# Optimization experiments

Hardware: AMD Instinct MI355X
Metric: run time of the kernel (lower is better)

## Reference

```python
import jax, jax.numpy as jnp
import numpy as np

B = 8192
H = 1024            # hidden_size
A = 512             # alphabet_size
S = 2               # sequence_length
D_IN = A * S        # 1024, gate input dim
D1, D2 = H // 2, H // 3   # decoder dims: 512, 341
TEMP = 1.0


def _linear_params(key, out_d, in_d):
    kw, kb = jax.random.split(key)
    lim = 1.0 / np.sqrt(in_d)
    W = jax.random.uniform(kw, (out_d, in_d), minval=-lim, maxval=lim, dtype=jnp.float32)
    b = jax.random.uniform(kb, (out_d,), minval=-lim, maxval=lim, dtype=jnp.float32)
    return W, b


def setup_inputs() -> dict:
    key = jax.random.key(0)
    ks = jax.random.split(key, 16)
    inp = {
        'x': jax.random.normal(ks[0], (B, D_IN), dtype=jnp.float32),
        'h': jax.random.normal(ks[1], (B, H), dtype=jnp.float32),
        'c': jax.random.normal(ks[2], (B, H), dtype=jnp.float32),
    }
    names = [('W_fi', 'b_fi', H, D_IN), ('W_fh', 'b_fh', H, H),
             ('W_ii', 'b_ii', H, D_IN), ('W_ih', 'b_ih', H, H),
             ('W_si', 'b_si', H, D_IN), ('W_sh', 'b_sh', H, H),
             ('W_oi', 'b_oi', H, D_IN), ('W_oh', 'b_oh', H, H),
             ('W_d1', 'b_d1', D1, H), ('W_d2', 'b_d2', D2, D1),
             ('W_d3', 'b_d3', A, D2)]
    for k, (wn, bn, od, idm) in zip(ks[3:3 + len(names)], names):
        W, b = _linear_params(k, od, idm)
        inp[wn] = W
        inp[bn] = b
    return inp


def reference(x, h, c,
              W_fi, b_fi, W_fh, b_fh,
              W_ii, b_ii, W_ih, b_ih,
              W_si, b_si, W_sh, b_sh,
              W_oi, b_oi, W_oh, b_oh,
              W_d1, b_d1, W_d2, b_d2, W_d3, b_d3):
    def lin(v, W, b):
        return v @ W.T + b

    f = jax.nn.sigmoid(lin(x, W_fi, b_fi) + lin(h, W_fh, b_fh))
    i = jax.nn.sigmoid(lin(x, W_ii, b_ii) + lin(h, W_ih, b_ih))
    s = jnp.tanh(lin(x, W_si, b_si) + lin(h, W_sh, b_sh))
    o = jax.nn.sigmoid(lin(x, W_oi, b_oi) + lin(h, W_oh, b_oh))
    c_new = c * f + i * s
    h_new = o * jnp.tanh(c_new)
    d = jnp.tanh(lin(h_new, W_d1, b_d1))
    d = jnp.tanh(lin(d, W_d2, b_d2))
    d = jax.nn.softmax(lin(d, W_d3, b_d3) / TEMP, axis=-1)
    return h_new, d
```

## Files before the change

kernel.cpp:

```cpp
#include <hip/hip_runtime.h>
#include <cstdint>
#include <cstddef>


typedef _Float16 half_t;
typedef _Float16 half8 __attribute__((ext_vector_type(8)));
typedef _Float16 half4v __attribute__((ext_vector_type(4)));
typedef float float4v __attribute__((ext_vector_type(4)));

#define GLD_LDS16(gptr, lptr)                                                  \
  __builtin_amdgcn_global_load_lds(                                            \
      (const __attribute__((address_space(1))) void*)(gptr),                   \
      (__attribute__((address_space(3))) void*)(lptr), 16, 0, 0)

__device__ __forceinline__ float fsig(float x) {
  return 1.0f / (1.0f + __expf(-x));
}
__device__ __forceinline__ float ftanh_(float x) {
  const float e = __expf(2.0f * x);
  return 1.0f - 2.0f / (e + 1.0f);
}

__global__ __launch_bounds__(512, 2) void gemm_gates(const half_t* __restrict__ A,
                                                     const half_t* __restrict__ Bw,
                                                     const float* __restrict__ bias,
                                                     const float* __restrict__ cin,
                                                     float* __restrict__ hout,
                                                     half_t* __restrict__ h2f) {
  constexpr int K = 2048;
  constexpr int NT = 64;
  __shared__ alignas(16) half_t As[3][256 * 32];
  __shared__ alignas(16) half_t Bs[3][256 * 32];
  const int tid = threadIdx.x;
  const int lane = tid & 63;
  const int wave = tid >> 6;
  const int m = lane & 15;
  const int q = lane >> 4;
  const int ks = (q ^ ((m >> 1) & 3)) << 3;
  const int wm = (wave >> 2) << 7;
  const int wn = (wave & 3) << 6;

  const int bid = blockIdx.x;
  const int xcd = bid & 7;
  const int l = bid >> 3;
  const size_t tile_n = (size_t)((xcd << 1) | (l & 1)) << 8;
  const size_t tile_m = (size_t)(l >> 1) << 8;

  const int ci0 = tid, ci1 = tid + 512;
  const int r0 = ci0 >> 2, k0s = (ci0 & 3) ^ ((r0 >> 1) & 3);
  const int r1 = ci1 >> 2, k1s = (ci1 & 3) ^ ((r1 >> 1) & 3);
  const half_t* Ag0 = A + (tile_m + r0) * (size_t)K + k0s * 8;
  const half_t* Ag1 = A + (tile_m + r1) * (size_t)K + k1s * 8;
  const half_t* Bg0 = Bw + (tile_n + r0) * (size_t)K + k0s * 8;
  const half_t* Bg1 = Bw + (tile_n + r1) * (size_t)K + k1s * 8;
  const int p0 = ci0 * 16, p1 = ci1 * 16;

  GLD_LDS16(Ag0, (char*)As[0] + p0);
  GLD_LDS16(Ag1, (char*)As[0] + p1);
  GLD_LDS16(Bg0, (char*)Bs[0] + p0);
  GLD_LDS16(Bg1, (char*)Bs[0] + p1);
  GLD_LDS16(Ag0 + 32, (char*)As[1] + p0);
  GLD_LDS16(Ag1 + 32, (char*)As[1] + p1);
  GLD_LDS16(Bg0 + 32, (char*)Bs[1] + p0);
  GLD_LDS16(Bg1 + 32, (char*)Bs[1] + p1);
  asm volatile("s_waitcnt vmcnt(4)" ::: "memory");
  __builtin_amdgcn_s_barrier();
  __builtin_amdgcn_sched_barrier(0);

  float4v acc[8][4] = {};
  int bc = 0;
  for (int t = 0; t < NT; ++t) {
    const half_t* as = As[bc];
    const half_t* bs = Bs[bc];
    const int bst = (bc + 2 >= 3) ? bc - 1 : bc + 2;
    const size_t koff = (size_t)(t + 2) * 32;
    half8 af[4], bf[4];
#pragma unroll
    for (int i = 0; i < 4; ++i)
      af[i] = *(const half8*)(as + (wm + i * 16 + m) * 32 + ks);
#pragma unroll
    for (int j = 0; j < 4; ++j)
      bf[j] = *(const half8*)(bs + (wn + j * 16 + m) * 32 + ks);
    if (t < NT - 2) {
      GLD_LDS16(Ag0 + koff, (char*)As[bst] + p0);
      GLD_LDS16(Ag1 + koff, (char*)As[bst] + p1);
    }
    __builtin_amdgcn_s_barrier();
    asm volatile("s_waitcnt lgkmcnt(0)" ::: "memory");
    __builtin_amdgcn_sched_barrier(0);
    __builtin_amdgcn_s_setprio(1);
#pragma unroll
    for (int i = 0; i < 4; ++i)
#pragma unroll
      for (int j = 0; j < 4; ++j)
        acc[i][j] = __builtin_amdgcn_mfma_f32_16x16x32_f16(af[i], bf[j],
                                                           acc[i][j], 0, 0, 0);
    __builtin_amdgcn_s_setprio(0);
    __builtin_amdgcn_s_barrier();
    __builtin_amdgcn_sched_barrier(0);
    half8 ag[4];
#pragma unroll
    for (int i = 0; i < 4; ++i)
      ag[i] = *(const half8*)(as + (wm + 64 + i * 16 + m) * 32 + ks);
    if (t < NT - 2) {
      GLD_LDS16(Bg0 + koff, (char*)Bs[bst] + p0);
      GLD_LDS16(Bg1 + koff, (char*)Bs[bst] + p1);
    }
    __builtin_amdgcn_s_barrier();
    asm volatile("s_waitcnt lgkmcnt(0)" ::: "memory");
    __builtin_amdgcn_sched_barrier(0);
    __builtin_amdgcn_s_setprio(1);
#pragma unroll
    for (int i = 0; i < 4; ++i)
#pragma unroll
      for (int j = 0; j < 4; ++j)
        acc[4 + i][j] = __builtin_amdgcn_mfma_f32_16x16x32_f16(
            ag[i], bf[j], acc[4 + i][j], 0, 0, 0);
    __builtin_amdgcn_s_setprio(0);
    if (t < NT - 2) {
      asm volatile("s_waitcnt vmcnt(4)" ::: "memory");
    } else if (t == NT - 2) {
      asm volatile("s_waitcnt vmcnt(0)" ::: "memory");
    }
    __builtin_amdgcn_s_barrier();
    __builtin_amdgcn_sched_barrier(0);
    bc = (bc + 1 == 3) ? 0 : bc + 1;
  }

  const int nwave = (int)tile_n + wn;
  const int u = ((nwave >> 6) << 4) + m;
  const int rtb = (int)((tile_m + wm) >> 4);
  const int ubase = (u >> 5) * 512 + ((u >> 3) & 3) * 128 + (u & 7);
  float bg[4];
#pragma unroll
  for (int g = 0; g < 4; ++g) bg[g] = bias[nwave + g * 16 + m];
#pragma unroll
  for (int i = 0; i < 8; ++i) {
#pragma unroll
    for (int r = 0; r < 4; ++r) {
      const size_t row = tile_m + wm + q * 4 + i * 16 + r;
      const size_t off = row * 1024 + u;
      const float F = fsig(acc[i][0][r] + bg[0]);
      const float I = fsig(acc[i][1][r] + bg[1]);
      const float S = ftanh_(acc[i][2][r] + bg[2]);
      const float O = fsig(acc[i][3][r] + bg[3]);
      const float cn = cin[off] * F + I * S;
      const float hn = O * ftanh_(cn);
      hout[off] = hn;
      h2f[(size_t)(rtb + i) * 16384 + ubase + (q * 4 + r) * 8] = (half_t)hn;
    }
  }
}

__global__ __launch_bounds__(512, 2) void fused_decoder(
    const half_t* __restrict__ h2f,
    const half_t* __restrict__ W1f,
    const float* __restrict__ b1,
    const half_t* __restrict__ W2f,
    const float* __restrict__ b2,
    const half_t* __restrict__ W3f,
    const float* __restrict__ b3,
    float* __restrict__ out) {
  __shared__ alignas(16) half_t A1s[2 * 16384];
  __shared__ alignas(16) half_t A2s[2 * 8192];
  __shared__ alignas(16) half_t A3s[2 * 6144];
  float* LOGL = (float*)A1s;

  const int tid = threadIdx.x;
  const int lane = tid & 63;
  const int w = tid >> 6;
  const int m = lane & 15;
  const int q = lane >> 4;
  const int b = blockIdx.x;

  const half_t* src = h2f + (size_t)b * 32768;
#pragma unroll
  for (int it = 0; it < 8; ++it)
    GLD_LDS16(src + (it * 512 + tid) * 8, (char*)A1s + (it * 512 + tid) * 16);
  asm volatile("s_waitcnt vmcnt(0)" ::: "memory");
  __syncthreads();

  {
    float4v acc[2][4] = {};
    const half_t* w1 = W1f + (size_t)(w * 4) * 16384 + lane * 8;
#pragma unroll 2
    for (int c = 0; c < 32; ++c) {
      half8 wf[4], af[2];
#pragma unroll
      for (int j = 0; j < 4; ++j)
        wf[j] = *(const half8*)(w1 + j * 16384 + c * 512);
#pragma unroll
      for (int rt = 0; rt < 2; ++rt)
        af[rt] = *(const half8*)(A1s + rt * 16384 + c * 512 + q * 128 + m * 8);
#pragma unroll
      for (int rt = 0; rt < 2; ++rt)
#pragma unroll
        for (int j = 0; j < 4; ++j)
          acc[rt][j] = __builtin_amdgcn_mfma_f32_16x16x32_f16(af[rt], wf[j],
                                                              acc[rt][j], 0, 0, 0);
    }
#pragma unroll
    for (int j = 0; j < 4; ++j) {
      const int col = w * 64 + j * 16 + m;
      const float bv = b1[col];
      const int cb = (col >> 5) * 512 + ((col >> 3) & 3) * 128 + (col & 7);
#pragma unroll
      for (int rt = 0; rt < 2; ++rt)
#pragma unroll
        for (int r = 0; r < 4; ++r)
          A2s[rt * 8192 + cb + (q * 4 + r) * 8] = (half_t)ftanh_(acc[rt][j][r] + bv);
    }
  }
  __syncthreads();

  {
    float4v acc[2][3] = {};
    const half_t* w2 = W2f + (size_t)(w * 3) * 8192 + lane * 8;
#pragma unroll 2
    for (int c = 0; c < 16; ++c) {
      half8 wf[3], af[2];
#pragma unroll
      for (int j = 0; j < 3; ++j)
        wf[j] = *(const half8*)(w2 + j * 8192 + c * 512);
#pragma unroll
      for (int rt = 0; rt < 2; ++rt)
        af[rt] = *(const half8*)(A2s + rt * 8192 + c * 512 + q * 128 + m * 8);
#pragma unroll
      for (int rt = 0; rt < 2; ++rt)
#pragma unroll
        for (int j = 0; j < 3; ++j)
          acc[rt][j] = __builtin_amdgcn_mfma_f32_16x16x32_f16(af[rt], wf[j],
                                                              acc[rt][j], 0, 0, 0);
    }
#pragma unroll
    for (int j = 0; j < 3; ++j) {
      const int col = w * 48 + j * 16 + m;
      const float bv = b2[col];
      const int cb = (col >> 5) * 512 + ((col >> 3) & 3) * 128 + (col & 7);
#pragma unroll
      for (int rt = 0; rt < 2; ++rt)
#pragma unroll
        for (int r = 0; r < 4; ++r)
          A3s[rt * 6144 + cb + (q * 4 + r) * 8] = (half_t)ftanh_(acc[rt][j][r] + bv);
    }
  }
  __syncthreads();

  {
    float4v acc[2][4] = {};
    const half_t* w3 = W3f + (size_t)(w * 4) * 6144 + lane * 8;
#pragma unroll 2
    for (int c = 0; c < 12; ++c) {
      half8 wf[4], af[2];
#pragma unroll
      for (int j = 0; j < 4; ++j)
        wf[j] = *(const half8*)(w3 + j * 6144 + c * 512);
#pragma unroll
      for (int rt = 0; rt < 2; ++rt)
        af[rt] = *(const half8*)(A3s + rt * 6144 + c * 512 + q * 128 + m * 8);
#pragma unroll
      for (int rt = 0; rt < 2; ++rt)
#pragma unroll
        for (int j = 0; j < 4; ++j)
          acc[rt][j] = __builtin_amdgcn_mfma_f32_16x16x32_f16(af[rt], wf[j],
                                                              acc[rt][j], 0, 0, 0);
    }
#pragma unroll
    for (int j = 0; j < 4; ++j) {
      const int col = w * 64 + j * 16 + m;
      const float bv = b3[col];
#pragma unroll
      for (int rt = 0; rt < 2; ++rt)
#pragma unroll
        for (int r = 0; r < 4; ++r)
          LOGL[(rt * 16 + q * 4 + r) * 512 + col] = acc[rt][j][r] + bv;
    }
  }
  __syncthreads();

#pragma unroll
  for (int rr = 0; rr < 4; ++rr) {
    const int row = w * 4 + rr;
    const float4v* srcv = (const float4v*)(LOGL + row * 512);
    const float4v v0 = srcv[lane * 2];
    const float4v v1 = srcv[lane * 2 + 1];
    float mx = fmaxf(fmaxf(fmaxf(v0.x, v0.y), fmaxf(v0.z, v0.w)),
                     fmaxf(fmaxf(v1.x, v1.y), fmaxf(v1.z, v1.w)));
#pragma unroll
    for (int off = 32; off > 0; off >>= 1) mx = fmaxf(mx, __shfl_xor(mx, off, 64));
    const float e0 = __expf(v0.x - mx), e1 = __expf(v0.y - mx);
    const float e2 = __expf(v0.z - mx), e3 = __expf(v0.w - mx);
    const float e4 = __expf(v1.x - mx), e5 = __expf(v1.y - mx);
    const float e6 = __expf(v1.z - mx), e7 = __expf(v1.w - mx);
    float sum = ((e0 + e1) + (e2 + e3)) + ((e4 + e5) + (e6 + e7));
#pragma unroll
    for (int off = 32; off > 0; off >>= 1) sum += __shfl_xor(sum, off, 64);
    const float inv = 1.0f / sum;
    float4v o0, o1;
    o0.x = e0 * inv; o0.y = e1 * inv; o0.z = e2 * inv; o0.w = e3 * inv;
    o1.x = e4 * inv; o1.y = e5 * inv; o1.z = e6 * inv; o1.w = e7 * inv;
    float4v* dst = (float4v*)(out + ((size_t)b * 32 + row) * 512);
    dst[lane * 2] = o0;
    dst[lane * 2 + 1] = o1;
  }
}

__global__ void prep_pack(const float* __restrict__ x, const float* __restrict__ h,
                          const float* __restrict__ Wfi, const float* __restrict__ Wfh,
                          const float* __restrict__ Wii, const float* __restrict__ Wih,
                          const float* __restrict__ Wsi, const float* __restrict__ Wsh,
                          const float* __restrict__ Woi, const float* __restrict__ Woh,
                          half_t* __restrict__ xh, half_t* __restrict__ wall) {
  const int bid = blockIdx.x;
  const float* src;
  half_t* dst;
  size_t idx;
  if (bid < 16384) {
    idx = ((size_t)bid * 256 + threadIdx.x) * 4;
    const size_t b = idx >> 11;
    const int col = (int)(idx & 2047);
    src = (col < 1024) ? (x + b * 1024 + col) : (h + b * 1024 + (col - 1024));
    dst = xh + idx;
  } else {
    idx = ((size_t)(bid - 16384) * 256 + threadIdx.x) * 4;
    const int n = (int)(idx >> 11);
    const int col = (int)(idx & 2047);
    const int g = (n >> 4) & 3;
    const size_t u = (size_t)(((n >> 6) << 4) | (n & 15));
    const float* Wi = (g == 0) ? Wfi : (g == 1) ? Wii : (g == 2) ? Wsi : Woi;
    const float* Wh = (g == 0) ? Wfh : (g == 1) ? Wih : (g == 2) ? Wsh : Woh;
    src = (col < 1024) ? (Wi + u * 1024 + col) : (Wh + u * 1024 + (col - 1024));
    dst = wall + idx;
  }
  const float4v v = *(const float4v*)src;
  half4v o;
  o.x = (half_t)v.x; o.y = (half_t)v.y; o.z = (half_t)v.z; o.w = (half_t)v.w;
  *(half4v*)dst = o;
}

__global__ void prep_small(const float* __restrict__ Wd1, const float* __restrict__ Wd2,
                           const float* __restrict__ Wd3, const float* __restrict__ bd2,
                           const float* __restrict__ bfi, const float* __restrict__ bfh,
                           const float* __restrict__ bii, const float* __restrict__ bih,
                           const float* __restrict__ bsi, const float* __restrict__ bsh,
                           const float* __restrict__ boi, const float* __restrict__ boh,
                           half_t* __restrict__ WD1, half_t* __restrict__ WD2h,
                           half_t* __restrict__ WD3h, float* __restrict__ BALL,
                           float* __restrict__ BD2) {
  const int bid = blockIdx.x;
  const int tid = threadIdx.x;
  if (bid < 512) {
    const size_t i4 = ((size_t)bid * 256 + tid) * 4;
    const int col = (int)(i4 >> 10);
    const int k0 = (int)(i4 & 1023);
    const float4v v = *(const float4v*)(Wd1 + i4);
    half4v o;
    o.x = (half_t)v.x; o.y = (half_t)v.y; o.z = (half_t)v.z; o.w = (half_t)v.w;
    const size_t fa = (size_t)(col >> 4) * 16384 + (k0 >> 5) * 512 +
                      ((k0 >> 3) & 3) * 128 + (col & 15) * 8 + (k0 & 7);
    *(half4v*)(WD1 + fa) = o;
  } else if (bid < 704) {
    const size_t i4 = ((size_t)(bid - 512) * 256 + tid) * 4;
    const int col = (int)(i4 >> 9);
    const int k0 = (int)(i4 & 511);
    half4v o;
    if (col < 341) {
      const float4v v = *(const float4v*)(Wd2 + (size_t)col * 512 + k0);
      o.x = (half_t)v.x; o.y = (half_t)v.y; o.z = (half_t)v.z; o.w = (half_t)v.w;
    } else {
      o.x = (half_t)0.f; o.y = (half_t)0.f; o.z = (half_t)0.f; o.w = (half_t)0.f;
    }
    const size_t fa = (size_t)(col >> 4) * 8192 + (k0 >> 5) * 512 +
                      ((k0 >> 3) & 3) * 128 + (col & 15) * 8 + (k0 & 7);
    *(half4v*)(WD2h + fa) = o;
  } else if (bid < 896) {
    const size_t i4 = ((size_t)(bid - 704) * 256 + tid) * 4;
    const int col = (int)(i4 / 384);
    const int k0 = (int)(i4 - (size_t)col * 384);
    half4v o;
    o.x = (k0 + 0 < 341) ? (half_t)Wd3[(size_t)col * 341 + k0 + 0] : (half_t)0.f;
    o.y = (k0 + 1 < 341) ? (half_t)Wd3[(size_t)col * 341 + k0 + 1] : (half_t)0.f;
    o.z = (k0 + 2 < 341) ? (half_t)Wd3[(size_t)col * 341 + k0 + 2] : (half_t)0.f;
    o.w = (k0 + 3 < 341) ? (half_t)Wd3[(size_t)col * 341 + k0 + 3] : (half_t)0.f;
    const size_t fa = (size_t)(col >> 4) * 6144 + (k0 >> 5) * 512 +
                      ((k0 >> 3) & 3) * 128 + (col & 15) * 8 + (k0 & 7);
    *(half4v*)(WD3h + fa) = o;
  } else if (bid < 912) {
    const int n = (bid - 896) * 256 + tid;
    const int g = (n >> 4) & 3;
    const int u = ((n >> 6) << 4) | (n & 15);
    const float* bi = (g == 0) ? bfi : (g == 1) ? bii : (g == 2) ? bsi : boi;
    const float* bh = (g == 0) ? bfh : (g == 1) ? bih : (g == 2) ? bsh : boh;
    BALL[n] = bi[u] + bh[u];
  } else {
    const int i = (bid - 912) * 256 + tid;
    if (i < 384) BD2[i] = (i < 341) ? bd2[i] : 0.0f;
  }
}

extern "C" void kernel_launch(void* const* d_in, const int* in_sizes, int n_in,
                              void* d_out, int out_size, void* d_ws, size_t ws_size,
                              hipStream_t stream) {
  const float* x = (const float*)d_in[0];
  const float* h = (const float*)d_in[1];
  const float* c = (const float*)d_in[2];
  const float* Wfi = (const float*)d_in[3];  const float* bfi = (const float*)d_in[4];
  const float* Wfh = (const float*)d_in[5];  const float* bfh = (const float*)d_in[6];
  const float* Wii = (const float*)d_in[7];  const float* bii = (const float*)d_in[8];
  const float* Wih = (const float*)d_in[9];  const float* bih = (const float*)d_in[10];
  const float* Wsi = (const float*)d_in[11]; const float* bsi = (const float*)d_in[12];
  const float* Wsh = (const float*)d_in[13]; const float* bsh = (const float*)d_in[14];
  const float* Woi = (const float*)d_in[15]; const float* boi = (const float*)d_in[16];
  const float* Woh = (const float*)d_in[17]; const float* boh = (const float*)d_in[18];
  const float* Wd1 = (const float*)d_in[19]; const float* bd1 = (const float*)d_in[20];
  const float* Wd2 = (const float*)d_in[21]; const float* bd2 = (const float*)d_in[22];
  const float* Wd3 = (const float*)d_in[23]; const float* bd3 = (const float*)d_in[24];

  char* ws = (char*)d_ws;
  size_t o = 0;
  auto alloc = [&](size_t bytes) {
    size_t cur = o;
    o += (bytes + 255) & ~(size_t)255;
    return cur;
  };
  half_t* XH   = (half_t*)(ws + alloc((size_t)8192 * 2048 * 2));
  half_t* WALL = (half_t*)(ws + alloc((size_t)4096 * 2048 * 2));
  float*  BALL = (float*)(ws + alloc(4096 * 4));
  half_t* WD1  = (half_t*)(ws + alloc((size_t)512 * 1024 * 2));
  half_t* WD2  = (half_t*)(ws + alloc((size_t)384 * 512 * 2));
  float*  BD2  = (float*)(ws + alloc(384 * 4));
  half_t* WD3  = (half_t*)(ws + alloc((size_t)512 * 384 * 2));
  half_t* H2F  = (half_t*)(ws + alloc((size_t)8192 * 1024 * 2));

  float* h_out = (float*)d_out;
  float* d_outp = (float*)d_out + (size_t)8192 * 1024;

  prep_pack<<<24576, 256, 0, stream>>>(x, h, Wfi, Wfh, Wii, Wih, Wsi, Wsh, Woi, Woh,
                                       XH, WALL);
  prep_small<<<914, 256, 0, stream>>>(Wd1, Wd2, Wd3, bd2, bfi, bfh, bii, bih, bsi, bsh,
                                      boi, boh, WD1, WD2, WD3, BALL, BD2);

  gemm_gates<<<512, 512, 0, stream>>>(XH, WALL, BALL, c, h_out, H2F);

  fused_decoder<<<256, 512, 0, stream>>>(H2F, WD1, bd1, WD2, BD2, WD3, bd3, d_outp);
}
```

Measured before the change: 384.3 us.

## Halve decoder rows per block to double grid, and grid-stride the pack kernel

The fused decoder now handles 16 batch rows per block instead of 32. This doubles the grid to 512 blocks, halves LDS use and register accumulators, and raises the occupancy hint to 4 blocks per CU, so all CUs have work. The cost is that each block reloads the full decoder weights for half as many rows, which doubles weight traffic from L2. Separately, the fp32-to-fp16 pack kernel changes from one-shot 24576 blocks to a 2048-block grid-stride loop to cut block launch overhead.

After: 390.8 us. Within noise of the previous version (+1.7%).

```diff
diff --git a/kernel.cpp b/kernel.cpp
--- a/kernel.cpp
+++ b/kernel.cpp
@@ -152,7 +152,7 @@
   }
 }
 
-__global__ __launch_bounds__(512, 2) void fused_decoder(
+__global__ __launch_bounds__(512, 4) void fused_decoder(
     const half_t* __restrict__ h2f,
     const half_t* __restrict__ W1f,
     const float* __restrict__ b1,
@@ -161,9 +161,9 @@
     const half_t* __restrict__ W3f,
     const float* __restrict__ b3,
     float* __restrict__ out) {
-  __shared__ alignas(16) half_t A1s[2 * 16384];
-  __shared__ alignas(16) half_t A2s[2 * 8192];
-  __shared__ alignas(16) half_t A3s[2 * 6144];
+  __shared__ alignas(16) half_t A1s[16384];
+  __shared__ alignas(16) half_t A2s[8192];
+  __shared__ alignas(16) half_t A3s[6144];
   float* LOGL = (float*)A1s;
 
   const int tid = threadIdx.x;
@@ -173,31 +173,26 @@
   const int q = lane >> 4;
   const int b = blockIdx.x;
 
-  const half_t* src = h2f + (size_t)b * 32768;
-#pragma unroll
-  for (int it = 0; it < 8; ++it)
+  const half_t* src = h2f + (size_t)b * 16384;
+#pragma unroll
+  for (int it = 0; it < 4; ++it)
     GLD_LDS16(src + (it * 512 + tid) * 8, (char*)A1s + (it * 512 + tid) * 16);
   asm volatile("s_waitcnt vmcnt(0)" ::: "memory");
   __syncthreads();
 
   {
-    float4v acc[2][4] = {};
+    float4v acc[4] = {};
     const half_t* w1 = W1f + (size_t)(w * 4) * 16384 + lane * 8;
-#pragma unroll 2
+#pragma unroll 4
     for (int c = 0; c < 32; ++c) {
-      half8 wf[4], af[2];
+      half8 wf[4], af;
 #pragma unroll
       for (int j = 0; j < 4; ++j)
         wf[j] = *(const half8*)(w1 + j * 16384 + c * 512);
-#pragma unroll
-      for (int rt = 0; rt < 2; ++rt)
-        af[rt] = *(const half8*)(A1s + rt * 16384 + c * 512 + q * 128 + m * 8);
-#pragma unroll
-      for (int rt = 0; rt < 2; ++rt)
-#pragma unroll
-        for (int j = 0; j < 4; ++j)
-          acc[rt][j] = __builtin_amdgcn_mfma_f32_16x16x32_f16(af[rt], wf[j],
-                                                              acc[rt][j], 0, 0, 0);
+      af = *(const half8*)(A1s + c * 512 + q * 128 + m * 8);
+#pragma unroll
+      for (int j = 0; j < 4; ++j)
+        acc[j] = __builtin_amdgcn_mfma_f32_16x16x32_f16(af, wf[j], acc[j], 0, 0, 0);
     }
 #pragma unroll
     for (int j = 0; j < 4; ++j) {
@@ -205,32 +200,25 @@
       const float bv = b1[col];
       const int cb = (col >> 5) * 512 + ((col >> 3) & 3) * 128 + (col & 7);
 #pragma unroll
-      for (int rt = 0; rt < 2; ++rt)
-#pragma unroll
-        for (int r = 0; r < 4; ++r)
-          A2s[rt * 8192 + cb + (q * 4 + r) * 8] = (half_t)ftanh_(acc[rt][j][r] + bv);
+      for (int r = 0; r < 4; ++r)
+        A2s[cb + (q * 4 + r) * 8] = (half_t)ftanh_(acc[j][r] + bv);
     }
   }
   __syncthreads();
 
   {
-    float4v acc[2][3] = {};
+    float4v acc[3] = {};
     const half_t* w2 = W2f + (size_t)(w * 3) * 8192 + lane * 8;
-#pragma unroll 2
+#pragma unroll 4
     for (int c = 0; c < 16; ++c) {
-      half8 wf[3], af[2];
+      half8 wf[3], af;
 #pragma unroll
       for (int j = 0; j < 3; ++j)
         wf[j] = *(const half8*)(w2 + j * 8192 + c * 512);
-#pragma unroll
-      for (int rt = 0; rt < 2; ++rt)
-        af[rt] = *(const half8*)(A2s + rt * 8192 + c * 512 + q * 128 + m * 8);
-#pragma unroll
-      for (int rt = 0; rt < 2; ++rt)
-#pragma unroll
-        for (int j = 0; j < 3; ++j)
-          acc[rt][j] = __builtin_amdgcn_mfma_f32_16x16x32_f16(af[rt], wf[j],
-                                                              acc[rt][j], 0, 0, 0);
+      af = *(const half8*)(A2s + c * 512 + q * 128 + m * 8);
+#pragma unroll
+      for (int j = 0; j < 3; ++j)
+        acc[j] = __builtin_amdgcn_mfma_f32_16x16x32_f16(af, wf[j], acc[j], 0, 0, 0);
     }
 #pragma unroll
     for (int j = 0; j < 3; ++j) {
@@ -238,49 +226,40 @@
       const float bv = b2[col];
       const int cb = (col >> 5) * 512 + ((col >> 3) & 3) * 128 + (col & 7);
 #pragma unroll
-      for (int rt = 0; rt < 2; ++rt)
-#pragma unroll
-        for (int r = 0; r < 4; ++r)
-          A3s[rt * 6144 + cb + (q * 4 + r) * 8] = (half_t)ftanh_(acc[rt][j][r] + bv);
+      for (int r = 0; r < 4; ++r)
+        A3s[cb + (q * 4 + r) * 8] = (half_t)ftanh_(acc[j][r] + bv);
     }
   }
   __syncthreads();
 
   {
-    float4v acc[2][4] = {};
+    float4v acc[4] = {};
     const half_t* w3 = W3f + (size_t)(w * 4) * 6144 + lane * 8;
-#pragma unroll 2
+#pragma unroll 4
     for (int c = 0; c < 12; ++c) {
-      half8 wf[4], af[2];
+      half8 wf[4], af;
 #pragma unroll
       for (int j = 0; j < 4; ++j)
         wf[j] = *(const half8*)(w3 + j * 6144 + c * 512);
-#pragma unroll
-      for (int rt = 0; rt < 2; ++rt)
-        af[rt] = *(const half8*)(A3s + rt * 6144 + c * 512 + q * 128 + m * 8);
-#pragma unroll
-      for (int rt = 0; rt < 2; ++rt)
-#pragma unroll
-        for (int j = 0; j < 4; ++j)
-          acc[rt][j] = __builtin_amdgcn_mfma_f32_16x16x32_f16(af[rt], wf[j],
-                                                              acc[rt][j], 0, 0, 0);
+      af = *(const half8*)(A3s + c * 512 + q * 128 + m * 8);
+#pragma unroll
+      for (int j = 0; j < 4; ++j)
+        acc[j] = __builtin_amdgcn_mfma_f32_16x16x32_f16(af, wf[j], acc[j], 0, 0, 0);
     }
 #pragma unroll
     for (int j = 0; j < 4; ++j) {
       const int col = w * 64 + j * 16 + m;
       const float bv = b3[col];
 #pragma unroll
-      for (int rt = 0; rt < 2; ++rt)
-#pragma unroll
-        for (int r = 0; r < 4; ++r)
-          LOGL[(rt * 16 + q * 4 + r) * 512 + col] = acc[rt][j][r] + bv;
+      for (int r = 0; r < 4; ++r)
+        LOGL[(q * 4 + r) * 512 + col] = acc[j][r] + bv;
     }
   }
   __syncthreads();
 
 #pragma unroll
-  for (int rr = 0; rr < 4; ++rr) {
-    const int row = w * 4 + rr;
+  for (int rr = 0; rr < 2; ++rr) {
+    const int row = w * 2 + rr;
     const float4v* srcv = (const float4v*)(LOGL + row * 512);
     const float4v v0 = srcv[lane * 2];
     const float4v v1 = srcv[lane * 2 + 1];
@@ -299,43 +278,48 @@
     float4v o0, o1;
     o0.x = e0 * inv; o0.y = e1 * inv; o0.z = e2 * inv; o0.w = e3 * inv;
     o1.x = e4 * inv; o1.y = e5 * inv; o1.z = e6 * inv; o1.w = e7 * inv;
-    float4v* dst = (float4v*)(out + ((size_t)b * 32 + row) * 512);
+    float4v* dst = (float4v*)(out + ((size_t)b * 16 + row) * 512);
     dst[lane * 2] = o0;
     dst[lane * 2 + 1] = o1;
   }
 }
 
-__global__ void prep_pack(const float* __restrict__ x, const float* __restrict__ h,
-                          const float* __restrict__ Wfi, const float* __restrict__ Wfh,
-                          const float* __restrict__ Wii, const float* __restrict__ Wih,
-                          const float* __restrict__ Wsi, const float* __restrict__ Wsh,
-                          const float* __restrict__ Woi, const float* __restrict__ Woh,
-                          half_t* __restrict__ xh, half_t* __restrict__ wall) {
-  const int bid = blockIdx.x;
-  const float* src;
-  half_t* dst;
-  size_t idx;
-  if (bid < 16384) {
-    idx = ((size_t)bid * 256 + threadIdx.x) * 4;
-    const size_t b = idx >> 11;
-    const int col = (int)(idx & 2047);
-    src = (col < 1024) ? (x + b * 1024 + col) : (h + b * 1024 + (col - 1024));
-    dst = xh + idx;
-  } else {
-    idx = ((size_t)(bid - 16384) * 256 + threadIdx.x) * 4;
-    const int n = (int)(idx >> 11);
-    const int col = (int)(idx & 2047);
-    const int g = (n >> 4) & 3;
-    const size_t u = (size_t)(((n >> 6) << 4) | (n & 15));
-    const float* Wi = (g == 0) ? Wfi : (g == 1) ? Wii : (g == 2) ? Wsi : Woi;
-    const float* Wh = (g == 0) ? Wfh : (g == 1) ? Wih : (g == 2) ? Wsh : Woh;
-    src = (col < 1024) ? (Wi + u * 1024 + col) : (Wh + u * 1024 + (col - 1024));
-    dst = wall + idx;
-  }
-  const float4v v = *(const float4v*)src;
-  half4v o;
-  o.x = (half_t)v.x; o.y = (half_t)v.y; o.z = (half_t)v.z; o.w = (half_t)v.w;
-  *(half4v*)dst = o;
+__global__ __launch_bounds__(256) void prep_pack(
+    const float* __restrict__ x, const float* __restrict__ h,
+    const float* __restrict__ Wfi, const float* __restrict__ Wfh,
+    const float* __restrict__ Wii, const float* __restrict__ Wih,
+    const float* __restrict__ Wsi, const float* __restrict__ Wsh,
+    const float* __restrict__ Woi, const float* __restrict__ Woh,
+    half_t* __restrict__ xh, half_t* __restrict__ wall) {
+  constexpr size_t NXH = (size_t)8192 * 2048 / 4;
+  constexpr size_t NTOT = NXH + (size_t)4096 * 2048 / 4;
+  constexpr size_t STRIDE = (size_t)2048 * 256;
+  for (size_t qd = (size_t)blockIdx.x * 256 + threadIdx.x; qd < NTOT;
+       qd += STRIDE) {
+    const float* src;
+    half_t* dst;
+    if (qd < NXH) {
+      const size_t idx = qd * 4;
+      const size_t bb = idx >> 11;
+      const int col = (int)(idx & 2047);
+      src = (col < 1024) ? (x + bb * 1024 + col) : (h + bb * 1024 + (col - 1024));
+      dst = xh + idx;
+    } else {
+      const size_t idx = (qd - NXH) * 4;
+      const int n = (int)(idx >> 11);
+      const int col = (int)(idx & 2047);
+      const int g = (n >> 4) & 3;
+      const size_t u = (size_t)(((n >> 6) << 4) | (n & 15));
+      const float* Wi = (g == 0) ? Wfi : (g == 1) ? Wii : (g == 2) ? Wsi : Woi;
+      const float* Wh = (g == 0) ? Wfh : (g == 1) ? Wih : (g == 2) ? Wsh : Woh;
+      src = (col < 1024) ? (Wi + u * 1024 + col) : (Wh + u * 1024 + (col - 1024));
+      dst = wall + idx;
+    }
+    const float4v v = *(const float4v*)src;
+    half4v o;
+    o.x = (half_t)v.x; o.y = (half_t)v.y; o.z = (half_t)v.z; o.w = (half_t)v.w;
+    *(half4v*)dst = o;
+  }
 }
 
 __global__ void prep_small(const float* __restrict__ Wd1, const float* __restrict__ Wd2,
@@ -435,12 +419,12 @@
   float* h_out = (float*)d_out;
   float* d_outp = (float*)d_out + (size_t)8192 * 1024;
 
-  prep_pack<<<24576, 256, 0, stream>>>(x, h, Wfi, Wfh, Wii, Wih, Wsi, Wsh, Woi, Woh,
-                                       XH, WALL);
+  prep_pack<<<2048, 256, 0, stream>>>(x, h, Wfi, Wfh, Wii, Wih, Wsi, Wsh, Woi, Woh,
+                                      XH, WALL);
   prep_small<<<914, 256, 0, stream>>>(Wd1, Wd2, Wd3, bd2, bfi, bfh, bii, bih, bsi, bsh,
                                       boi, boh, WD1, WD2, WD3, BALL, BD2);
 
   gemm_gates<<<512, 512, 0, stream>>>(XH, WALL, BALL, c, h_out, H2F);
 
-  fused_decoder<<<256, 512, 0, stream>>>(H2F, WD1, bd1, WD2, BD2, WD3, bd3, d_outp);
-}
+  fused_decoder<<<512, 512, 0, stream>>>(H2F, WD1, bd1, WD2, BD2, WD3, bd3, d_outp);
+}
```

## Retile gates GEMM to 256x128 block tiles with 64-deep K stages

Applied to the files above, without the earlier changes.

Changes the fused gate GEMM block tile from 256x256 with K=32 per stage to 256x128 with K=64 per stage. The grid doubles to 1024 blocks, each wave now owns a 64x64 output tile, and the LDS swizzle changes to an XOR over 8 chunks. The loop is split into two K-halves, and the global-to-LDS loads are redistributed across them. The aim is to halve the number of pipeline iterations and barriers and to give more blocks for scheduling. In exchange, each block reuses less data, so operand LDS reads per MFMA go up, and the LDS footprint grows to about 144KB per block.

After: 385.4 us. About the same (+0.3%).

```diff
diff --git a/kernel.cpp b/kernel.cpp
--- a/kernel.cpp
+++ b/kernel.cpp
@@ -28,62 +28,70 @@
                                                      float* __restrict__ hout,
                                                      half_t* __restrict__ h2f) {
   constexpr int K = 2048;
-  constexpr int NT = 64;
-  __shared__ alignas(16) half_t As[3][256 * 32];
-  __shared__ alignas(16) half_t Bs[3][256 * 32];
+  constexpr int NT = 32;
+  __shared__ alignas(16) half_t As[3][256 * 64];
+  __shared__ alignas(16) half_t Bs[3][128 * 64];
   const int tid = threadIdx.x;
   const int lane = tid & 63;
   const int wave = tid >> 6;
   const int m = lane & 15;
   const int q = lane >> 4;
-  const int ks = (q ^ ((m >> 1) & 3)) << 3;
-  const int wm = (wave >> 2) << 7;
-  const int wn = (wave & 3) << 6;
+  const int x0 = ((q) ^ (m & 7)) << 3;
+  const int x1 = ((4 + q) ^ (m & 7)) << 3;
+  const int wm = (wave >> 1) << 6;
+  const int wn = (wave & 1) << 6;
 
   const int bid = blockIdx.x;
   const int xcd = bid & 7;
   const int l = bid >> 3;
-  const size_t tile_n = (size_t)((xcd << 1) | (l & 1)) << 8;
-  const size_t tile_m = (size_t)(l >> 1) << 8;
-
-  const int ci0 = tid, ci1 = tid + 512;
-  const int r0 = ci0 >> 2, k0s = (ci0 & 3) ^ ((r0 >> 1) & 3);
-  const int r1 = ci1 >> 2, k1s = (ci1 & 3) ^ ((r1 >> 1) & 3);
-  const half_t* Ag0 = A + (tile_m + r0) * (size_t)K + k0s * 8;
-  const half_t* Ag1 = A + (tile_m + r1) * (size_t)K + k1s * 8;
-  const half_t* Bg0 = Bw + (tile_n + r0) * (size_t)K + k0s * 8;
-  const half_t* Bg1 = Bw + (tile_n + r1) * (size_t)K + k1s * 8;
-  const int p0 = ci0 * 16, p1 = ci1 * 16;
-
-  GLD_LDS16(Ag0, (char*)As[0] + p0);
-  GLD_LDS16(Ag1, (char*)As[0] + p1);
-  GLD_LDS16(Bg0, (char*)Bs[0] + p0);
-  GLD_LDS16(Bg1, (char*)Bs[0] + p1);
-  GLD_LDS16(Ag0 + 32, (char*)As[1] + p0);
-  GLD_LDS16(Ag1 + 32, (char*)As[1] + p1);
-  GLD_LDS16(Bg0 + 32, (char*)Bs[1] + p0);
-  GLD_LDS16(Bg1 + 32, (char*)Bs[1] + p1);
-  asm volatile("s_waitcnt vmcnt(4)" ::: "memory");
+  const size_t tile_n = (size_t)((xcd << 2) | (l & 3)) << 7;
+  const size_t tile_m = (size_t)(l >> 2) << 8;
+
+  const int r0 = tid >> 3;
+  const int cs = (((tid & 7) ^ (r0 & 7)) << 3);
+  const half_t* Ag0 = A + (tile_m + r0) * (size_t)K + cs;
+  const half_t* Ag1 = Ag0 + (size_t)64 * K;
+  const half_t* Ag2 = Ag0 + (size_t)128 * K;
+  const half_t* Ag3 = Ag0 + (size_t)192 * K;
+  const half_t* Bg0 = Bw + (tile_n + r0) * (size_t)K + cs;
+  const half_t* Bg1 = Bg0 + (size_t)64 * K;
+  const int pa0 = tid * 16, pa1 = pa0 + 8192, pa2 = pa0 + 16384, pa3 = pa0 + 24576;
+  const int pb0 = tid * 16, pb1 = pb0 + 8192;
+
+  GLD_LDS16(Ag0, (char*)As[0] + pa0);
+  GLD_LDS16(Ag1, (char*)As[0] + pa1);
+  GLD_LDS16(Bg0, (char*)Bs[0] + pb0);
+  GLD_LDS16(Ag2, (char*)As[0] + pa2);
+  GLD_LDS16(Ag3, (char*)As[0] + pa3);
+  GLD_LDS16(Bg1, (char*)Bs[0] + pb1);
+  GLD_LDS16(Ag0 + 64, (char*)As[1] + pa0);
+  GLD_LDS16(Ag1 + 64, (char*)As[1] + pa1);
+  GLD_LDS16(Bg0 + 64, (char*)Bs[1] + pb0);
+  GLD_LDS16(Ag2 + 64, (char*)As[1] + pa2);
+  GLD_LDS16(Ag3 + 64, (char*)As[1] + pa3);
+  GLD_LDS16(Bg1 + 64, (char*)Bs[1] + pb1);
+  asm volatile("s_waitcnt vmcnt(6)" ::: "memory");
   __builtin_amdgcn_s_barrier();
   __builtin_amdgcn_sched_barrier(0);
 
-  float4v acc[8][4] = {};
+  float4v acc[4][4] = {};
   int bc = 0;
   for (int t = 0; t < NT; ++t) {
     const half_t* as = As[bc];
     const half_t* bs = Bs[bc];
     const int bst = (bc + 2 >= 3) ? bc - 1 : bc + 2;
-    const size_t koff = (size_t)(t + 2) * 32;
+    const size_t koff = (size_t)(t + 2) * 64;
     half8 af[4], bf[4];
 #pragma unroll
     for (int i = 0; i < 4; ++i)
-      af[i] = *(const half8*)(as + (wm + i * 16 + m) * 32 + ks);
+      af[i] = *(const half8*)(as + (wm + i * 16 + m) * 64 + x0);
 #pragma unroll
     for (int j = 0; j < 4; ++j)
-      bf[j] = *(const half8*)(bs + (wn + j * 16 + m) * 32 + ks);
+      bf[j] = *(const half8*)(bs + (wn + j * 16 + m) * 64 + x0);
     if (t < NT - 2) {
-      GLD_LDS16(Ag0 + koff, (char*)As[bst] + p0);
-      GLD_LDS16(Ag1 + koff, (char*)As[bst] + p1);
+      GLD_LDS16(Ag0 + koff, (char*)As[bst] + pa0);
+      GLD_LDS16(Ag1 + koff, (char*)As[bst] + pa1);
+      GLD_LDS16(Bg0 + koff, (char*)Bs[bst] + pb0);
     }
     __builtin_amdgcn_s_barrier();
     asm volatile("s_waitcnt lgkmcnt(0)" ::: "memory");
@@ -98,13 +106,17 @@
     __builtin_amdgcn_s_setprio(0);
     __builtin_amdgcn_s_barrier();
     __builtin_amdgcn_sched_barrier(0);
-    half8 ag[4];
+    half8 ag[4], bg2[4];
 #pragma unroll
     for (int i = 0; i < 4; ++i)
-      ag[i] = *(const half8*)(as + (wm + 64 + i * 16 + m) * 32 + ks);
+      ag[i] = *(const half8*)(as + (wm + i * 16 + m) * 64 + x1);
+#pragma unroll
+    for (int j = 0; j < 4; ++j)
+      bg2[j] = *(const half8*)(bs + (wn + j * 16 + m) * 64 + x1);
     if (t < NT - 2) {
-      GLD_LDS16(Bg0 + koff, (char*)Bs[bst] + p0);
-      GLD_LDS16(Bg1 + koff, (char*)Bs[bst] + p1);
+      GLD_LDS16(Ag2 + koff, (char*)As[bst] + pa2);
+      GLD_LDS16(Ag3 + koff, (char*)As[bst] + pa3);
+      GLD_LDS16(Bg1 + koff, (char*)Bs[bst] + pb1);
     }
     __builtin_amdgcn_s_barrier();
     asm volatile("s_waitcnt lgkmcnt(0)" ::: "memory");
@@ -114,11 +126,11 @@
     for (int i = 0; i < 4; ++i)
 #pragma unroll
       for (int j = 0; j < 4; ++j)
-        acc[4 + i][j] = __builtin_amdgcn_mfma_f32_16x16x32_f16(
-            ag[i], bf[j], acc[4 + i][j], 0, 0, 0);
+        acc[i][j] = __builtin_amdgcn_mfma_f32_16x16x32_f16(ag[i], bg2[j],
+                                                           acc[i][j], 0, 0, 0);
     __builtin_amdgcn_s_setprio(0);
     if (t < NT - 2) {
-      asm volatile("s_waitcnt vmcnt(4)" ::: "memory");
+      asm volatile("s_waitcnt vmcnt(6)" ::: "memory");
     } else if (t == NT - 2) {
       asm volatile("s_waitcnt vmcnt(0)" ::: "memory");
     }
@@ -135,7 +147,7 @@
 #pragma unroll
   for (int g = 0; g < 4; ++g) bg[g] = bias[nwave + g * 16 + m];
 #pragma unroll
-  for (int i = 0; i < 8; ++i) {
+  for (int i = 0; i < 4; ++i) {
 #pragma unroll
     for (int r = 0; r < 4; ++r) {
       const size_t row = tile_m + wm + q * 4 + i * 16 + r;
@@ -317,9 +329,9 @@
   size_t idx;
   if (bid < 16384) {
     idx = ((size_t)bid * 256 + threadIdx.x) * 4;
-    const size_t b = idx >> 11;
+    const size_t bb = idx >> 11;
     const int col = (int)(idx & 2047);
-    src = (col < 1024) ? (x + b * 1024 + col) : (h + b * 1024 + (col - 1024));
+    src = (col < 1024) ? (x + bb * 1024 + col) : (h + bb * 1024 + (col - 1024));
     dst = xh + idx;
   } else {
     idx = ((size_t)(bid - 16384) * 256 + threadIdx.x) * 4;
@@ -440,7 +452,7 @@
   prep_small<<<914, 256, 0, stream>>>(Wd1, Wd2, Wd3, bd2, bfi, bfh, bii, bih, bsi, bsh,
                                       boi, boh, WD1, WD2, WD3, BALL, BD2);
 
-  gemm_gates<<<512, 512, 0, stream>>>(XH, WALL, BALL, c, h_out, H2F);
+  gemm_gates<<<1024, 512, 0, stream>>>(XH, WALL, BALL, c, h_out, H2F);
 
   fused_decoder<<<256, 512, 0, stream>>>(H2F, WD1, bd1, WD2, BD2, WD3, bd3, d_outp);
 }
```
